# Kernel optimization log

Measured on AMD Instinct MI355X. Metric: run time of the kernel, lower is better.

## Reference

```python
import jax, jax.numpy as jnp
import numpy as np

E, DM, DH, K, DIL = 8, 512, 1024, 3, 2
N, L = 128, 128
PAD = DIL * (K - 1) // 2  # 'same' padding


def _conv1d(x, w):
    # x: [N, Cin, L], w: [Cout, Cin, K] -> [N, Cout, L]
    return jax.lax.conv_general_dilated(
        x, w, window_strides=(1,), padding=[(PAD, PAD)],
        rhs_dilation=(DIL,), dimension_numbers=("NCH", "OIH", "NCH"))


def _moe_conv(x, W, B, onehot):
    # W: [E, Cout, Cin, K], B: [E, Cout], onehot: [N, E]
    ys = jax.vmap(lambda w, b: _conv1d(x, w) + b[None, :, None])(W, B)  # [E, N, Cout, L]
    return jnp.einsum("enol,ne->nol", ys, onehot)


def setup_inputs() -> dict:
    key = jax.random.key(0)
    k1, k2, k3, k4, k5 = jax.random.split(key, 5)
    inp = jax.random.normal(k1, (N, DM, L), dtype=jnp.float32)
    # uneven per-expert sample counts summing to N (samples pre-sorted by expert)
    fwd_expert_count = jnp.asarray(np.array([10, 20, 16, 16, 12, 22, 14, 18], dtype=np.int32))
    w1 = jax.random.normal(k2, (E, DH, DM, K), dtype=jnp.float32) * 0.02
    b1 = jax.random.normal(k3, (E, DH), dtype=jnp.float32) * 0.02
    w2 = jax.random.normal(k4, (E, DM, DH, K), dtype=jnp.float32) * 0.02
    b2 = jax.random.normal(k5, (E, DM), dtype=jnp.float32) * 0.02
    return {"inp": inp, "fwd_expert_count": fwd_expert_count,
            "w1": w1, "b1": b1, "w2": w2, "b2": b2}


def reference(inp, fwd_expert_count, w1, b1, w2, b2):
    # map each sample index to its expert via cumulative counts
    cs = jnp.cumsum(fwd_expert_count)
    eid = jnp.searchsorted(cs, jnp.arange(N), side="right")  # [N]
    onehot = (eid[:, None] == jnp.arange(E)[None, :]).astype(inp.dtype)  # [N, E]
    h = _moe_conv(inp, w1, b1, onehot)       # [N, DH, L]
    h = jax.nn.gelu(h)
    out = _moe_conv(h, w2, b2, onehot)       # [N, DM, L]
    return out
```

## Files before the change

### kernel.cpp

```cpp
#include <hip/hip_runtime.h>
#include <hip/hip_bf16.h>
#include <stdint.h>


typedef __attribute__((ext_vector_type(8))) short short8;
typedef __attribute__((ext_vector_type(4))) float f32x4;

#define DMV 512
#define DHV 1024

#define OFF_X   0ull
#define OFF_H   (16ull << 20)
#define OFF_W1  (48ull << 20)
#define OFF_W2  (72ull << 20)

#define VMW(n) asm volatile("s_waitcnt vmcnt(" #n ")" ::: "memory")
#define VMNOP  do {} while (0)

__device__ __forceinline__ uint16_t f2bf(float f) {
  uint32_t u = __builtin_bit_cast(uint32_t, f);
  uint32_t r = (u + 0x7FFFu + ((u >> 16) & 1u)) >> 16;
  return (uint16_t)r;
}

__device__ __forceinline__ void async_copy16(const void* g, void* l) {
  __builtin_amdgcn_global_load_lds(
      (const __attribute__((address_space(1))) uint32_t*)g,
      (__attribute__((address_space(3))) uint32_t*)l, 16, 0, 0);
}

__device__ __forceinline__ float gelu_f(float x) {
  float u = 0.7978845608028654f * (x + 0.044715f * x * x * x);
  float t = __expf(2.0f * u);
  float th = 1.0f - 2.0f / (t + 1.0f);
  return 0.5f * x * (1.0f + th);
}

__global__ __launch_bounds__(256) void prep_x_t(const float* __restrict__ inp,
                                                uint16_t* __restrict__ xp) {
  uint32_t b = blockIdx.x;
  uint32_t s = b >> 4, cc = b & 15u;
  __shared__ uint16_t xs[32][132];
  uint32_t t = threadIdx.x;
  const float* src0 = inp + ((size_t)s * DMV + cc * 32u) * 128u;
#pragma unroll
  for (int i = 0; i < 4; ++i) {
    uint32_t idx = (uint32_t)i * 256u + t;
    uint32_t ch = idx >> 5, l4 = idx & 31u;
    float4 f = *(const float4*)(src0 + ch * 128u + l4 * 4u);
    uint2 pk;
    pk.x = (uint32_t)f2bf(f.x) | ((uint32_t)f2bf(f.y) << 16);
    pk.y = (uint32_t)f2bf(f.z) | ((uint32_t)f2bf(f.w) << 16);
    *(uint2*)&xs[ch][l4 * 4u] = pk;
  }
  __syncthreads();
  uint32_t l = t >> 1, half = t & 1u;
  uint32_t fl = ((l + 2u) >> 1) & 3u;
#pragma unroll
  for (int hi = 0; hi < 2; ++hi) {
    uint32_t sub = half * 2u + (uint32_t)hi;
    uint32_t cg = (sub ^ fl) & 3u;
    uint32_t pk[4];
#pragma unroll
    for (int p2 = 0; p2 < 4; ++p2) {
      uint32_t c0 = cg * 8u + (uint32_t)p2 * 2u;
      pk[p2] = (uint32_t)xs[c0][l] | ((uint32_t)xs[c0 + 1][l] << 16);
    }
    uint4 v; v.x = pk[0]; v.y = pk[1]; v.z = pk[2]; v.w = pk[3];
    size_t slot = (((size_t)s * 16u + cc) * 128u + l) * 4u + sub;
    *(uint4*)(xp + slot * 8u) = v;
  }
}

template <int LOGCG, int LOGO>
__global__ __launch_bounds__(256) void prep_w_c(const float* __restrict__ w,
                                                uint16_t* __restrict__ wp) {
  constexpr uint32_t C = 4u << LOGCG;
  constexpr uint32_t CCn = C >> 5;
  constexpr uint32_t MTn = 1u << (LOGO - 7);
  uint32_t t = blockIdx.x * 256u + threadIdx.x;
  uint32_t cg = t & ((1u << LOGCG) - 1u);
  uint32_t o = (t >> LOGCG) & ((1u << LOGO) - 1u);
  uint32_t e = t >> (LOGCG + LOGO);
  uint32_t row = o & 127u, mt = o >> 7;
  const float* src = w + (((size_t)(e << LOGO) + o) * C + cg * 4u) * 3u;
  float4 f0 = *(const float4*)(src);
  float4 f1 = *(const float4*)(src + 4);
  float4 f2 = *(const float4*)(src + 8);
  uint32_t cc = cg >> 3;
  uint32_t sub = ((cg >> 1) & 3u) ^ ((row >> 1) & 3u);
  uint32_t j0 = (cg & 1u) * 4u;
  size_t base = (((size_t)e * CCn + cc) * MTn + mt) * 3u;
  uint2 q;
  q.x = (uint32_t)f2bf(f0.x) | ((uint32_t)f2bf(f0.w) << 16);
  q.y = (uint32_t)f2bf(f1.z) | ((uint32_t)f2bf(f2.y) << 16);
  *(uint2*)(wp + ((base + 0u) * 128u + row) * 32u + sub * 8u + j0) = q;
  q.x = (uint32_t)f2bf(f0.y) | ((uint32_t)f2bf(f1.x) << 16);
  q.y = (uint32_t)f2bf(f1.w) | ((uint32_t)f2bf(f2.z) << 16);
  *(uint2*)(wp + ((base + 1u) * 128u + row) * 32u + sub * 8u + j0) = q;
  q.x = (uint32_t)f2bf(f0.z) | ((uint32_t)f2bf(f1.y) << 16);
  q.y = (uint32_t)f2bf(f2.x) | ((uint32_t)f2bf(f2.w) << 16);
  *(uint2*)(wp + ((base + 2u) * 128u + row) * 32u + sub * 8u + j0) = q;
}

#define PHASE_STEP(K, HH, READB, STAGE_BODY, VM_BODY)                          \
  {                                                                            \
    short8 af_[4];                                                             \
    _Pragma("unroll") for (int q = 0; q < 4; ++q)                              \
      af_[q] = *(const short8*)(br + aOff[(HH) * 4 + q] + (uint32_t)(K) * 8192u); \
    if (READB) {                                                               \
      _Pragma("unroll") for (int bq = 0; bq < 4; ++bq) {                       \
        uint32_t r_ = lB[bq] + 2u * (uint32_t)(K);                             \
        bfk[bq] = *(const short8*)(br + pOff + r_ * 64u +                      \
                    (((uint32_t)kg ^ (r_ >> 1)) & 3u) * 16u);                  \
      }                                                                        \
    }                                                                          \
    STAGE_BODY;                                                                \
    VM_BODY;                                                                   \
    __builtin_amdgcn_s_barrier();                                              \
    asm volatile("s_waitcnt lgkmcnt(0)" ::: "memory");                         \
    __builtin_amdgcn_s_setprio(1);                                             \
    _Pragma("unroll") for (int q = 0; q < 4; ++q)                              \
      _Pragma("unroll") for (int bq = 0; bq < 4; ++bq)                         \
        acc[(HH) * 4 + q][bq] = __builtin_amdgcn_mfma_f32_16x16x32_bf16(       \
            af_[q], bfk[bq], acc[(HH) * 4 + q][bq], 0, 0, 0);                  \
    __builtin_amdgcn_s_setprio(0);                                             \
    __builtin_amdgcn_s_barrier();                                              \
  }

template <int PHASE>
__global__ __launch_bounds__(512, 2) void conv_mfma(
    const uint16_t* __restrict__ bprep, const uint16_t* __restrict__ wprep,
    const float* __restrict__ bias, const int* __restrict__ cnt,
    uint16_t* __restrict__ hout, float* __restrict__ fout) {
  constexpr int CC = (PHASE == 1) ? 16 : 32;
  constexpr int HALVES = (PHASE == 1) ? 2 : 1;
  constexpr int MTP = (PHASE == 1) ? 8 : 4;
  constexpr int AREP = 4 * HALVES;
  constexpr int OO = (PHASE == 1) ? DHV : DMV;
  constexpr uint32_t AS = HALVES * 24576u;
  constexpr uint32_t BUFS = AS + 16896u;

  uint32_t b = blockIdx.x;
  uint32_t work = (b & 7u) * 32u + (b >> 3);
  const int pr = work & 63;
  const int mt = work >> 6;
  int e = 0;
  {
    int cum = cnt[0];
    while (2 * pr >= cum && e < 7) { ++e; cum += cnt[e]; }
  }
  const int tid = threadIdx.x;
  const int lane = tid & 63;
  const int wv = tid >> 6;
  const int wr = wv >> 2, wc = wv & 3;
  const int l15 = lane & 15, kg = lane >> 4;

  __shared__ __align__(16) uint8_t lds[2 * BUFS];

  uint32_t aOff[AREP];
#pragma unroll
  for (int a = 0; a < AREP; ++a) {
    uint32_t ri = (HALVES == 2) ? (uint32_t)(a * 16 + l15)
                                : (uint32_t)(wr * 64 + a * 16 + l15);
    uint32_t base = (HALVES == 2) ? (uint32_t)wr * 24576u : 0u;
    aOff[a] = base + ri * 64u + (((uint32_t)kg ^ (ri >> 1)) & 3u) * 16u;
  }
  uint32_t lB[4];
#pragma unroll
  for (int bq = 0; bq < 4; ++bq) lB[bq] = (uint32_t)((wc & 1) * 64 + bq * 16 + l15);
  const uint32_t pOff = AS + (uint32_t)(wc >> 1) * 8448u;
  const int mtBase = (PHASE == 1) ? mt * 2 : mt;

  const uint16_t* wTile0 = wprep + ((size_t)e * CC * MTP + mtBase) * 12288;
  auto SA = [&](uint8_t* bw, int ccn, int h, int k) {
    async_copy16(wTile0 + (size_t)ccn * (MTP * 12288) + (h * 3 + k) * 4096 + tid * 8,
                 bw + (uint32_t)(h * 3 + k) * 8192u + (uint32_t)tid * 16);
  };
  auto SBL = [&](uint8_t* bw, int ccn, int p) {
    async_copy16(bprep + ((size_t)(2 * pr + p) * CC + ccn) * 4096 + tid * 8,
                 bw + AS + (uint32_t)p * 8448u + 128u + (uint32_t)tid * 16);
  };

  if (tid < 64) {
    uint32_t n = (uint32_t)tid >> 5, rest = (uint32_t)tid & 31u;
    uint32_t p = rest >> 4, ri = (rest >> 2) & 3u, sb = rest & 3u;
    uint32_t rowByte = (ri < 2) ? ri * 64u : (8320u + (ri - 2) * 64u);
    uint4 z = make_uint4(0, 0, 0, 0);
    *(uint4*)(lds + n * BUFS + AS + p * 8448u + rowByte + sb * 16u) = z;
  }
  asm volatile("s_waitcnt lgkmcnt(0)" ::: "memory");

  if (PHASE == 1) {
    SBL(lds, 0, 0); SBL(lds, 0, 1);
    SA(lds, 0, 0, 0); SA(lds, 0, 1, 0);
    SA(lds, 0, 0, 1); SA(lds, 0, 1, 1);
    SA(lds, 0, 0, 2); SA(lds, 0, 1, 2);
    VMW(4);
  } else {
    SBL(lds, 0, 0); SBL(lds, 0, 1);
    SA(lds, 0, 0, 0); SA(lds, 0, 0, 1); SA(lds, 0, 0, 2);
    VMW(2);
  }
  __builtin_amdgcn_s_barrier();

  f32x4 acc[AREP][4] = {};
  short8 bfk[4];

  if (PHASE == 1) {
#pragma unroll 1
    for (int cc = 0; cc < CC - 1; ++cc) {
      const uint8_t* br = lds + (uint32_t)(cc & 1) * BUFS;
      uint8_t* bw = lds + (uint32_t)((cc & 1) ^ 1) * BUFS;
      const int cn = cc + 1;
      PHASE_STEP(0, 0, true,  { SBL(bw, cn, 0); SBL(bw, cn, 1); }, VMNOP);
      PHASE_STEP(0, 1, false, { SA(bw, cn, 0, 0); SA(bw, cn, 1, 0); }, VMW(6));
      PHASE_STEP(1, 0, true,  { SA(bw, cn, 0, 1); }, VMNOP);
      PHASE_STEP(1, 1, false, { SA(bw, cn, 1, 1); }, VMW(6));
      PHASE_STEP(2, 0, true,  { SA(bw, cn, 0, 2); }, VMNOP);
      PHASE_STEP(2, 1, false, { SA(bw, cn, 1, 2); }, VMW(4));
    }
    {
      const uint8_t* br = lds + (uint32_t)((CC - 1) & 1) * BUFS;
      PHASE_STEP(0, 0, true,  {}, VMNOP);
      PHASE_STEP(0, 1, false, {}, VMW(2));
      PHASE_STEP(1, 0, true,  {}, VMNOP);
      PHASE_STEP(1, 1, false, {}, VMW(0));
      PHASE_STEP(2, 0, true,  {}, VMNOP);
      PHASE_STEP(2, 1, false, {}, VMNOP);
    }
  } else {
#pragma unroll 1
    for (int cc = 0; cc < CC - 1; ++cc) {
      const uint8_t* br = lds + (uint32_t)(cc & 1) * BUFS;
      uint8_t* bw = lds + (uint32_t)((cc & 1) ^ 1) * BUFS;
      const int cn = cc + 1;
      PHASE_STEP(0, 0, true, { SBL(bw, cn, 0); SBL(bw, cn, 1); SA(bw, cn, 0, 0); }, VMW(4));
      PHASE_STEP(1, 0, true, { SA(bw, cn, 0, 1); }, VMW(4));
      PHASE_STEP(2, 0, true, { SA(bw, cn, 0, 2); }, VMW(2));
    }
    {
      const uint8_t* br = lds + (uint32_t)((CC - 1) & 1) * BUFS;
      PHASE_STEP(0, 0, true, {}, VMW(1));
      PHASE_STEP(1, 0, true, {}, VMW(0));
      PHASE_STEP(2, 0, true, {}, VMNOP);
    }
  }

  const int p = wc >> 1;
  const int s = 2 * pr + p;
  if (PHASE == 1) {
#pragma unroll
    for (int a = 0; a < AREP; ++a) {
      int ob = mt * 256 + wr * 128 + a * 16 + kg * 4;
      float4 bv = *(const float4*)(bias + (size_t)e * OO + ob);
      int cc2 = mt * 8 + wr * 4 + (a >> 1);
      uint32_t g = (uint32_t)((a & 1) * 2 + (kg >> 1));
      uint32_t j0 = (uint32_t)((kg & 1) * 4);
#pragma unroll
      for (int bq = 0; bq < 4; ++bq) {
        int l = (wc & 1) * 64 + bq * 16 + l15;
        uint32_t flq = ((uint32_t)(l + 2) >> 1) & 3u;
        uint32_t sub = g ^ flq;
        float v0 = gelu_f(acc[a][bq][0] + bv.x);
        float v1 = gelu_f(acc[a][bq][1] + bv.y);
        float v2 = gelu_f(acc[a][bq][2] + bv.z);
        float v3 = gelu_f(acc[a][bq][3] + bv.w);
        uint2 pk;
        pk.x = (uint32_t)f2bf(v0) | ((uint32_t)f2bf(v1) << 16);
        pk.y = (uint32_t)f2bf(v2) | ((uint32_t)f2bf(v3) << 16);
        size_t ci = ((size_t)s * 32 + cc2) * 128 + l;
        *(uint2*)(hout + ci * 32 + sub * 8 + j0) = pk;
      }
    }
  } else {
#pragma unroll
    for (int a = 0; a < AREP; ++a) {
      int ob = mt * 128 + wr * 64 + a * 16 + kg * 4;
      float4 bv = *(const float4*)(bias + (size_t)e * OO + ob);
      float bvr[4] = {bv.x, bv.y, bv.z, bv.w};
      float* op = fout + ((size_t)s * DMV + ob) * 128;
#pragma unroll
      for (int bq = 0; bq < 4; ++bq) {
        int l = (wc & 1) * 64 + bq * 16 + l15;
#pragma unroll
        for (int r = 0; r < 4; ++r)
          op[(size_t)r * 128 + l] = acc[a][bq][r] + bvr[r];
      }
    }
  }
}

extern "C" void kernel_launch(void* const* d_in, const int* in_sizes, int n_in,
                              void* d_out, int out_size, void* d_ws, size_t ws_size,
                              hipStream_t stream) {
  const float* inp = (const float*)d_in[0];
  const int* cnt = (const int*)d_in[1];
  const float* w1 = (const float*)d_in[2];
  const float* b1 = (const float*)d_in[3];
  const float* w2 = (const float*)d_in[4];
  const float* b2 = (const float*)d_in[5];
  float* out = (float*)d_out;
  uint8_t* ws = (uint8_t*)d_ws;
  uint16_t* xp = (uint16_t*)(ws + OFF_X);
  uint16_t* hp = (uint16_t*)(ws + OFF_H);
  uint16_t* w1p = (uint16_t*)(ws + OFF_W1);
  uint16_t* w2p = (uint16_t*)(ws + OFF_W2);

  prep_x_t<<<dim3(2048), dim3(256), 0, stream>>>(inp, xp);
  prep_w_c<7, 10><<<dim3(4096), dim3(256), 0, stream>>>(w1, w1p);
  prep_w_c<8, 9><<<dim3(4096), dim3(256), 0, stream>>>(w2, w2p);
  conv_mfma<1><<<dim3(256), dim3(512), 0, stream>>>(xp, w1p, b1, cnt, hp, nullptr);
  conv_mfma<2><<<dim3(256), dim3(512), 0, stream>>>(hp, w2p, b2, cnt, nullptr, out);
}
```

Before: 140.8 us.

## Shrink conv tiles to one sample per block with 256-thread blocks

Each conv block now handles a single sample and a 128-channel output tile with 4 waves, instead of a sample pair with up to 256 output channels and 8 waves. This multiplies the grid size (1024 and 512 blocks) and unifies both phases into one pipeline, improving load balance and occupancy across CUs. The trade-off is less reuse of each weight tile per load: weights are re-fetched per sample rather than shared across two samples, which raises global and L2 traffic.

```diff
diff --git a/kernel.cpp b/kernel.cpp
--- a/kernel.cpp
+++ b/kernel.cpp
@@ -103,17 +103,15 @@
   *(uint2*)(wp + ((base + 2u) * 128u + row) * 32u + sub * 8u + j0) = q;
 }
 
-#define PHASE_STEP(K, HH, READB, STAGE_BODY, VM_BODY)                          \
+#define PHASE_STEP(K, STAGE_BODY, VM_BODY)                                     \
   {                                                                            \
-    short8 af_[4];                                                             \
+    short8 af_[4], bf_[4];                                                     \
     _Pragma("unroll") for (int q = 0; q < 4; ++q)                              \
-      af_[q] = *(const short8*)(br + aOff[(HH) * 4 + q] + (uint32_t)(K) * 8192u); \
-    if (READB) {                                                               \
-      _Pragma("unroll") for (int bq = 0; bq < 4; ++bq) {                       \
-        uint32_t r_ = lB[bq] + 2u * (uint32_t)(K);                             \
-        bfk[bq] = *(const short8*)(br + pOff + r_ * 64u +                      \
-                    (((uint32_t)kg ^ (r_ >> 1)) & 3u) * 16u);                  \
-      }                                                                        \
+      af_[q] = *(const short8*)(br + aOff[q] + (uint32_t)(K) * 8192u);         \
+    _Pragma("unroll") for (int bq = 0; bq < 4; ++bq) {                         \
+      uint32_t r_ = lB[bq] + 2u * (uint32_t)(K);                               \
+      bf_[bq] = *(const short8*)(br + 24576u + r_ * 64u +                      \
+                  (((uint32_t)kg ^ (r_ >> 1)) & 3u) * 16u);                    \
     }                                                                          \
     STAGE_BODY;                                                                \
     VM_BODY;                                                                   \
@@ -122,144 +120,104 @@
     __builtin_amdgcn_s_setprio(1);                                             \
     _Pragma("unroll") for (int q = 0; q < 4; ++q)                              \
       _Pragma("unroll") for (int bq = 0; bq < 4; ++bq)                         \
-        acc[(HH) * 4 + q][bq] = __builtin_amdgcn_mfma_f32_16x16x32_bf16(       \
-            af_[q], bfk[bq], acc[(HH) * 4 + q][bq], 0, 0, 0);                  \
+        acc[q][bq] = __builtin_amdgcn_mfma_f32_16x16x32_bf16(                  \
+            af_[q], bf_[bq], acc[q][bq], 0, 0, 0);                             \
     __builtin_amdgcn_s_setprio(0);                                             \
     __builtin_amdgcn_s_barrier();                                              \
   }
 
 template <int PHASE>
-__global__ __launch_bounds__(512, 2) void conv_mfma(
+__global__ __launch_bounds__(256, 2) void conv_mfma(
     const uint16_t* __restrict__ bprep, const uint16_t* __restrict__ wprep,
     const float* __restrict__ bias, const int* __restrict__ cnt,
     uint16_t* __restrict__ hout, float* __restrict__ fout) {
   constexpr int CC = (PHASE == 1) ? 16 : 32;
-  constexpr int HALVES = (PHASE == 1) ? 2 : 1;
   constexpr int MTP = (PHASE == 1) ? 8 : 4;
-  constexpr int AREP = 4 * HALVES;
   constexpr int OO = (PHASE == 1) ? DHV : DMV;
-  constexpr uint32_t AS = HALVES * 24576u;
-  constexpr uint32_t BUFS = AS + 16896u;
+  constexpr uint32_t BUFS = 24576u + 8448u;
 
   uint32_t b = blockIdx.x;
-  uint32_t work = (b & 7u) * 32u + (b >> 3);
-  const int pr = work & 63;
-  const int mt = work >> 6;
+  constexpr uint32_t CPX = (128u * MTP) >> 3;
+  uint32_t work = (b & 7u) * CPX + (b >> 3);
+  const int s = work & 127;
+  const int mt = work >> 7;
   int e = 0;
   {
     int cum = cnt[0];
-    while (2 * pr >= cum && e < 7) { ++e; cum += cnt[e]; }
+    while (s >= cum && e < 7) { ++e; cum += cnt[e]; }
   }
   const int tid = threadIdx.x;
   const int lane = tid & 63;
   const int wv = tid >> 6;
-  const int wr = wv >> 2, wc = wv & 3;
+  const int wr = wv >> 1, wc = wv & 1;
   const int l15 = lane & 15, kg = lane >> 4;
 
   __shared__ __align__(16) uint8_t lds[2 * BUFS];
 
-  uint32_t aOff[AREP];
-#pragma unroll
-  for (int a = 0; a < AREP; ++a) {
-    uint32_t ri = (HALVES == 2) ? (uint32_t)(a * 16 + l15)
-                                : (uint32_t)(wr * 64 + a * 16 + l15);
-    uint32_t base = (HALVES == 2) ? (uint32_t)wr * 24576u : 0u;
-    aOff[a] = base + ri * 64u + (((uint32_t)kg ^ (ri >> 1)) & 3u) * 16u;
+  uint32_t aOff[4];
+#pragma unroll
+  for (int a = 0; a < 4; ++a) {
+    uint32_t ri = (uint32_t)(wr * 64 + a * 16 + l15);
+    aOff[a] = ri * 64u + (((uint32_t)kg ^ (ri >> 1)) & 3u) * 16u;
   }
   uint32_t lB[4];
 #pragma unroll
-  for (int bq = 0; bq < 4; ++bq) lB[bq] = (uint32_t)((wc & 1) * 64 + bq * 16 + l15);
-  const uint32_t pOff = AS + (uint32_t)(wc >> 1) * 8448u;
-  const int mtBase = (PHASE == 1) ? mt * 2 : mt;
-
-  const uint16_t* wTile0 = wprep + ((size_t)e * CC * MTP + mtBase) * 12288;
-  auto SA = [&](uint8_t* bw, int ccn, int h, int k) {
-    async_copy16(wTile0 + (size_t)ccn * (MTP * 12288) + (h * 3 + k) * 4096 + tid * 8,
-                 bw + (uint32_t)(h * 3 + k) * 8192u + (uint32_t)tid * 16);
+  for (int bq = 0; bq < 4; ++bq) lB[bq] = (uint32_t)(wc * 64 + bq * 16 + l15);
+
+  const uint16_t* wTile0 = wprep + ((size_t)e * CC * MTP + mt) * 12288;
+  auto SA = [&](uint8_t* bw, int ccn, int k, int h) {
+    async_copy16(wTile0 + (size_t)ccn * (MTP * 12288) + k * 4096 + h * 2048 + tid * 8,
+                 bw + (uint32_t)k * 8192u + (uint32_t)h * 4096u + (uint32_t)tid * 16);
   };
-  auto SBL = [&](uint8_t* bw, int ccn, int p) {
-    async_copy16(bprep + ((size_t)(2 * pr + p) * CC + ccn) * 4096 + tid * 8,
-                 bw + AS + (uint32_t)p * 8448u + 128u + (uint32_t)tid * 16);
+  auto SBL = [&](uint8_t* bw, int ccn, int h) {
+    async_copy16(bprep + ((size_t)s * CC + ccn) * 4096 + h * 2048 + tid * 8,
+                 bw + 24576u + 128u + (uint32_t)h * 4096u + (uint32_t)tid * 16);
   };
 
-  if (tid < 64) {
-    uint32_t n = (uint32_t)tid >> 5, rest = (uint32_t)tid & 31u;
-    uint32_t p = rest >> 4, ri = (rest >> 2) & 3u, sb = rest & 3u;
+  if (tid < 32) {
+    uint32_t n = (uint32_t)tid >> 4, ri = ((uint32_t)tid >> 2) & 3u, sb = (uint32_t)tid & 3u;
     uint32_t rowByte = (ri < 2) ? ri * 64u : (8320u + (ri - 2) * 64u);
     uint4 z = make_uint4(0, 0, 0, 0);
-    *(uint4*)(lds + n * BUFS + AS + p * 8448u + rowByte + sb * 16u) = z;
-  }
+    *(uint4*)(lds + n * BUFS + 24576u + rowByte + sb * 16u) = z;
+  }
+
+  SBL(lds, 0, 0); SBL(lds, 0, 1);
+  SA(lds, 0, 0, 0); SA(lds, 0, 0, 1);
+  SA(lds, 0, 1, 0); SA(lds, 0, 1, 1);
+  SA(lds, 0, 2, 0); SA(lds, 0, 2, 1);
+  VMW(4);
   asm volatile("s_waitcnt lgkmcnt(0)" ::: "memory");
+  __builtin_amdgcn_s_barrier();
+
+  f32x4 acc[4][4] = {};
+
+#pragma unroll 1
+  for (int cc = 0; cc < CC - 1; ++cc) {
+    const uint8_t* br = lds + (uint32_t)(cc & 1) * BUFS;
+    uint8_t* bw = lds + (uint32_t)((cc & 1) ^ 1) * BUFS;
+    const int cn = cc + 1;
+    PHASE_STEP(0, { SBL(bw, cn, 0); SBL(bw, cn, 1); SA(bw, cn, 0, 0); SA(bw, cn, 0, 1); }, VMW(6));
+    PHASE_STEP(1, { SA(bw, cn, 1, 0); SA(bw, cn, 1, 1); }, VMW(6));
+    PHASE_STEP(2, { SA(bw, cn, 2, 0); SA(bw, cn, 2, 1); }, VMW(4));
+  }
+  {
+    const uint8_t* br = lds + (uint32_t)((CC - 1) & 1) * BUFS;
+    PHASE_STEP(0, {}, VMW(2));
+    PHASE_STEP(1, {}, VMW(0));
+    PHASE_STEP(2, {}, VMNOP);
+  }
 
   if (PHASE == 1) {
-    SBL(lds, 0, 0); SBL(lds, 0, 1);
-    SA(lds, 0, 0, 0); SA(lds, 0, 1, 0);
-    SA(lds, 0, 0, 1); SA(lds, 0, 1, 1);
-    SA(lds, 0, 0, 2); SA(lds, 0, 1, 2);
-    VMW(4);
-  } else {
-    SBL(lds, 0, 0); SBL(lds, 0, 1);
-    SA(lds, 0, 0, 0); SA(lds, 0, 0, 1); SA(lds, 0, 0, 2);
-    VMW(2);
-  }
-  __builtin_amdgcn_s_barrier();
-
-  f32x4 acc[AREP][4] = {};
-  short8 bfk[4];
-
-  if (PHASE == 1) {
-#pragma unroll 1
-    for (int cc = 0; cc < CC - 1; ++cc) {
-      const uint8_t* br = lds + (uint32_t)(cc & 1) * BUFS;
-      uint8_t* bw = lds + (uint32_t)((cc & 1) ^ 1) * BUFS;
-      const int cn = cc + 1;
-      PHASE_STEP(0, 0, true,  { SBL(bw, cn, 0); SBL(bw, cn, 1); }, VMNOP);
-      PHASE_STEP(0, 1, false, { SA(bw, cn, 0, 0); SA(bw, cn, 1, 0); }, VMW(6));
-      PHASE_STEP(1, 0, true,  { SA(bw, cn, 0, 1); }, VMNOP);
-      PHASE_STEP(1, 1, false, { SA(bw, cn, 1, 1); }, VMW(6));
-      PHASE_STEP(2, 0, true,  { SA(bw, cn, 0, 2); }, VMNOP);
-      PHASE_STEP(2, 1, false, { SA(bw, cn, 1, 2); }, VMW(4));
-    }
-    {
-      const uint8_t* br = lds + (uint32_t)((CC - 1) & 1) * BUFS;
-      PHASE_STEP(0, 0, true,  {}, VMNOP);
-      PHASE_STEP(0, 1, false, {}, VMW(2));
-      PHASE_STEP(1, 0, true,  {}, VMNOP);
-      PHASE_STEP(1, 1, false, {}, VMW(0));
-      PHASE_STEP(2, 0, true,  {}, VMNOP);
-      PHASE_STEP(2, 1, false, {}, VMNOP);
-    }
-  } else {
-#pragma unroll 1
-    for (int cc = 0; cc < CC - 1; ++cc) {
-      const uint8_t* br = lds + (uint32_t)(cc & 1) * BUFS;
-      uint8_t* bw = lds + (uint32_t)((cc & 1) ^ 1) * BUFS;
-      const int cn = cc + 1;
-      PHASE_STEP(0, 0, true, { SBL(bw, cn, 0); SBL(bw, cn, 1); SA(bw, cn, 0, 0); }, VMW(4));
-      PHASE_STEP(1, 0, true, { SA(bw, cn, 0, 1); }, VMW(4));
-      PHASE_STEP(2, 0, true, { SA(bw, cn, 0, 2); }, VMW(2));
-    }
-    {
-      const uint8_t* br = lds + (uint32_t)((CC - 1) & 1) * BUFS;
-      PHASE_STEP(0, 0, true, {}, VMW(1));
-      PHASE_STEP(1, 0, true, {}, VMW(0));
-      PHASE_STEP(2, 0, true, {}, VMNOP);
-    }
-  }
-
-  const int p = wc >> 1;
-  const int s = 2 * pr + p;
-  if (PHASE == 1) {
-#pragma unroll
-    for (int a = 0; a < AREP; ++a) {
-      int ob = mt * 256 + wr * 128 + a * 16 + kg * 4;
+#pragma unroll
+    for (int a = 0; a < 4; ++a) {
+      int ob = mt * 128 + wr * 64 + a * 16 + kg * 4;
       float4 bv = *(const float4*)(bias + (size_t)e * OO + ob);
-      int cc2 = mt * 8 + wr * 4 + (a >> 1);
+      int cc2 = mt * 4 + wr * 2 + (a >> 1);
       uint32_t g = (uint32_t)((a & 1) * 2 + (kg >> 1));
       uint32_t j0 = (uint32_t)((kg & 1) * 4);
 #pragma unroll
       for (int bq = 0; bq < 4; ++bq) {
-        int l = (wc & 1) * 64 + bq * 16 + l15;
+        int l = wc * 64 + bq * 16 + l15;
         uint32_t flq = ((uint32_t)(l + 2) >> 1) & 3u;
         uint32_t sub = g ^ flq;
         float v0 = gelu_f(acc[a][bq][0] + bv.x);
@@ -275,14 +233,14 @@
     }
   } else {
 #pragma unroll
-    for (int a = 0; a < AREP; ++a) {
+    for (int a = 0; a < 4; ++a) {
       int ob = mt * 128 + wr * 64 + a * 16 + kg * 4;
       float4 bv = *(const float4*)(bias + (size_t)e * OO + ob);
       float bvr[4] = {bv.x, bv.y, bv.z, bv.w};
       float* op = fout + ((size_t)s * DMV + ob) * 128;
 #pragma unroll
       for (int bq = 0; bq < 4; ++bq) {
-        int l = (wc & 1) * 64 + bq * 16 + l15;
+        int l = wc * 64 + bq * 16 + l15;
 #pragma unroll
         for (int r = 0; r < 4; ++r)
           op[(size_t)r * 128 + l] = acc[a][bq][r] + bvr[r];
@@ -310,6 +268,6 @@
   prep_x_t<<<dim3(2048), dim3(256), 0, stream>>>(inp, xp);
   prep_w_c<7, 10><<<dim3(4096), dim3(256), 0, stream>>>(w1, w1p);
   prep_w_c<8, 9><<<dim3(4096), dim3(256), 0, stream>>>(w2, w2p);
-  conv_mfma<1><<<dim3(256), dim3(512), 0, stream>>>(xp, w1p, b1, cnt, hp, nullptr);
-  conv_mfma<2><<<dim3(256), dim3(512), 0, stream>>>(hp, w2p, b2, cnt, nullptr, out);
-}
+  conv_mfma<1><<<dim3(1024), dim3(256), 0, stream>>>(xp, w1p, b1, cnt, hp, nullptr);
+  conv_mfma<2><<<dim3(512), dim3(256), 0, stream>>>(hp, w2p, b2, cnt, nullptr, out);
+}
```

Measured after the change: 142.1 us. About the same (+0.9%).
